# Performance work log

Hardware: AMD Instinct MI355X
Metric: run time of the kernel (lower is better)

The kernel has to match this reference:

```python
import jax, jax.numpy as jnp
import numpy as np

N_HEAD = 6


def setup_inputs() -> dict:
    key = jax.random.key(0)
    k1, k2, k3 = jax.random.split(key, 3)
    B, N, D = 16, 512, 768
    d_head = D // N_HEAD
    p_mask = jnp.ones((B, N), dtype=jnp.float32)
    feature = jax.random.normal(k1, (B, N, D), dtype=jnp.float32)
    # nn.Linear weights (out, in); scaled like torch default init
    W = jax.random.normal(k2, (D, D), dtype=jnp.float32) / np.sqrt(D)
    # attn Linear(2*d_head -> n_head); only the diagonal head rows are used
    Wa = jax.random.normal(k3, (N_HEAD, 2 * d_head), dtype=jnp.float32) / np.sqrt(2 * d_head)
    return {"p_mask": p_mask, "feature": feature, "W": W, "Wa": Wa, "num_layers": 2}


def reference(p_mask, feature, W, Wa, num_layers):
    B, N, D = feature.shape
    H = N_HEAD
    Dh = D // H
    # adj[b,q,k] = p_mask[b,q] * p_mask[b,k]  (bmm of unsqueezed mask)
    adj = p_mask[:, :, None] * p_mask[:, None, :]  # (B,N,N)
    mask = adj[:, :, :, None] > 0                   # (B,N,N,1)
    for _ in range(num_layers):
        residual = feature
        qk = (feature @ W.T).reshape(B, N, H, Dh)  # (B,N,H,Dh)
        # concat(q,k) @ Wa[h] decomposes into query part + key part
        sq = jnp.einsum('bqhd,hd->bqh', qk, Wa[:, :Dh])
        sk = jnp.einsum('bkhd,hd->bkh', qk, Wa[:, Dh:])
        score = jnp.tanh(sq[:, :, None, :] + sk[:, None, :, :])  # (B,N,N,H)
        # masked_fill with -1e-8 where adj == 0 (faithful to source)
        score = jnp.where(mask, score, jnp.float32(-1e-8))
        attn = jax.nn.softmax(score, axis=2)  # softmax over key dim (dim=-2)
        # dropout p=0 in eval -> identity
        hid = jnp.tanh(jnp.einsum('bqkh,bkhd->bqhd', attn, qk))  # (B,N,H,Dh)
        feature = residual + hid.reshape(B, N, D)
    return feature
```

## Files before the change

### kernel.cpp

```cpp
#include <hip/hip_runtime.h>
#include <hip/hip_bf16.h>
#include <stdint.h>

#define BATCH 16
#define NSEQ  512
#define DMODEL 768
#define NHEAD 6
#define DHEAD 128
#define MROWS (BATCH * NSEQ)
#define QBLK  32
#define KTILE 64

typedef __attribute__((ext_vector_type(8))) __bf16 bf16x8;
typedef __attribute__((ext_vector_type(4))) __bf16 bf16x4;
typedef __attribute__((ext_vector_type(4))) float  f32x4;
typedef __attribute__((ext_vector_type(4))) unsigned int u32x4;

#define GLD16(gp, lp) __builtin_amdgcn_global_load_lds( \
    (const __attribute__((address_space(1))) unsigned int*)(gp), \
    (__attribute__((address_space(3))) unsigned int*)(lp), 16, 0, 0)

#define BAR_PLAIN() do { asm volatile("" ::: "memory"); \
    __builtin_amdgcn_s_barrier(); asm volatile("" ::: "memory"); } while (0)
#define BAR_LGKM() do { asm volatile("s_waitcnt lgkmcnt(0)" ::: "memory"); \
    __builtin_amdgcn_s_barrier(); asm volatile("" ::: "memory"); } while (0)

__global__ void cvt_bf16_kernel(const float* __restrict__ src,
                                __bf16* __restrict__ dst, int n4) {
    int i = blockIdx.x * blockDim.x + threadIdx.x;
    if (i < n4) {
        float4 v = reinterpret_cast<const float4*>(src)[i];
        bf16x4 o;
        o.x = (__bf16)v.x; o.y = (__bf16)v.y; o.z = (__bf16)v.z; o.w = (__bf16)v.w;
        reinterpret_cast<bf16x4*>(dst)[i] = o;
    }
}

__global__ __launch_bounds__(256) void gemm_bt(const __bf16* __restrict__ A,
                                               const __bf16* __restrict__ Bm,
                                               __bf16* __restrict__ C,
                                               const float* __restrict__ Wa,
                                               const float* __restrict__ pmask,
                                               float* __restrict__ eq_t,
                                               float* __restrict__ ek_t) {
    __shared__ __align__(16) __bf16 As[2][64 * 32];
    __shared__ __align__(16) __bf16 Bs[2][128 * 32];
    const int tid  = threadIdx.x;
    const int lane = tid & 63;
    const int wave = tid >> 6;
    const int wm = wave >> 1, wn = wave & 1;

    const int wg  = blockIdx.x;
    const int nid = (wg & 7) * 96 + (wg >> 3);
    const int bx  = nid % 6;
    const int by  = nid / 6;
    const int m0 = by * 64;
    const int n0 = bx * 128;

    f32x4 acc[2][4] = {};

    const int e0   = tid * 8;
    const int row0 = tid >> 2;
    const int k0i  = (tid & 3) * 8;

    const int lr = lane & 15;
    const int lg = lane >> 4;
    const int kb = lg * 8;

    #define STAGE(kt, bufi) do { \
        GLD16(A  + (size_t)(m0 + row0)      * DMODEL + (kt) + k0i, &As[bufi][e0]); \
        GLD16(Bm + (size_t)(n0 + row0)      * DMODEL + (kt) + k0i, &Bs[bufi][e0]); \
        GLD16(Bm + (size_t)(n0 + row0 + 64) * DMODEL + (kt) + k0i, &Bs[bufi][e0 + 2048]); \
    } while (0)

    STAGE(0, 0);

    for (int t = 0; t < 24; t++) {
        const int buf = t & 1;
        if (t < 23) {
            STAGE((t + 1) * 32, buf ^ 1);
            asm volatile("s_waitcnt vmcnt(3)" ::: "memory");
        } else {
            asm volatile("s_waitcnt vmcnt(0)" ::: "memory");
        }
        __builtin_amdgcn_s_barrier();
        asm volatile("" ::: "memory");

        bf16x8 af[2], bfv[4];
        #pragma unroll
        for (int i = 0; i < 2; i++)
            af[i] = *reinterpret_cast<const bf16x8*>(&As[buf][(wm * 32 + i * 16 + lr) * 32 + kb]);
        #pragma unroll
        for (int j = 0; j < 4; j++)
            bfv[j] = *reinterpret_cast<const bf16x8*>(&Bs[buf][(wn * 64 + j * 16 + lr) * 32 + kb]);
        #pragma unroll
        for (int i = 0; i < 2; i++)
            #pragma unroll
            for (int j = 0; j < 4; j++)
                acc[i][j] = __builtin_amdgcn_mfma_f32_16x16x32_bf16(af[i], bfv[j], acc[i][j], 0, 0, 0);

        BAR_PLAIN();
    }
    #undef STAGE

    const int rg = lg * 4;
    #pragma unroll
    for (int i = 0; i < 2; i++) {
        #pragma unroll
        for (int j = 0; j < 4; j++) {
            #pragma unroll
            for (int r = 0; r < 4; r++) {
                int row = m0 + wm * 32 + i * 16 + rg + r;
                int col = n0 + wn * 64 + j * 16 + lr;
                C[(size_t)row * DMODEL + col] = (__bf16)acc[i][j][r];
            }
        }
    }

    const int h = bx;
    float wqv[4], wkv[4];
    #pragma unroll
    for (int j = 0; j < 4; j++) {
        int d = wn * 64 + j * 16 + lr;
        wqv[j] = Wa[h * 256 + d];
        wkv[j] = Wa[h * 256 + 128 + d];
    }
    float* red = reinterpret_cast<float*>(&As[0][0]);
    #pragma unroll
    for (int i = 0; i < 2; i++) {
        #pragma unroll
        for (int r = 0; r < 4; r++) {
            float aq = 0.f, ak = 0.f;
            #pragma unroll
            for (int j = 0; j < 4; j++) {
                aq += acc[i][j][r] * wqv[j];
                ak += acc[i][j][r] * wkv[j];
            }
            #pragma unroll
            for (int off = 1; off < 16; off <<= 1) {
                aq += __shfl_xor(aq, off);
                ak += __shfl_xor(ak, off);
            }
            if (lr == 0) {
                int row = wm * 32 + i * 16 + rg + r;
                red[(0 * 64 + row) * 2 + wn] = aq;
                red[(1 * 64 + row) * 2 + wn] = ak;
            }
        }
    }
    __syncthreads();
    if (tid < 64) {
        int row = m0 + tid;
        float s = red[tid * 2] + red[tid * 2 + 1];
        eq_t[(size_t)h * MROWS + row] = (pmask[row] > 0.f) ? __expf(2.f * s) : 0.f;
    } else if (tid < 128) {
        int rl  = tid - 64;
        int row = m0 + rl;
        float s = red[(64 + rl) * 2] + red[(64 + rl) * 2 + 1];
        ek_t[(size_t)h * MROWS + row] = (pmask[row] > 0.f) ? __expf(2.f * s) : 0.f;
    }
}

__global__ __launch_bounds__(256) void attn_pv(const __bf16* __restrict__ QK,
                                               const float* __restrict__ eq_t,
                                               const float* __restrict__ ek_t,
                                               const float* __restrict__ residual,
                                               float* __restrict__ out,
                                               __bf16* __restrict__ out_bf) {
    const int wg  = blockIdx.x;
    const int nid = (wg & 7) * 192 + (wg >> 3);
    const int qt = nid & 15;
    const int hb = nid >> 4;
    const int h  = hb % NHEAD;
    const int b  = hb / NHEAD;
    const int q0 = qt * QBLK;

    __shared__ __align__(16) __bf16 w[QBLK][512];
    __shared__ __align__(16) __bf16 Vt[2][DHEAD * KTILE];
    const int tid  = threadIdx.x;
    const int lane = tid & 63;
    const int wave = tid >> 6;

    const int wd0 = wave * 32;
    const int lr  = lane & 15;
    const int lg  = lane >> 4;

    const int sd0 = (tid & 15) * 8;
    const int sk0 = (tid >> 4) * 4;
    const __bf16* Vbase = QK + (size_t)b * NSEQ * DMODEL + (size_t)h * DHEAD + sd0;

    u32x4 A0, A1, A2, A3, B0, B1, B2, B3;
    #define LOADS(S0, S1, S2, S3, t) do { \
        const __bf16* p = Vbase + (size_t)((t) * KTILE + sk0) * DMODEL; \
        S0 = *reinterpret_cast<const u32x4*>(p); \
        S1 = *reinterpret_cast<const u32x4*>(p + DMODEL); \
        S2 = *reinterpret_cast<const u32x4*>(p + 2 * DMODEL); \
        S3 = *reinterpret_cast<const u32x4*>(p + 3 * DMODEL); \
    } while (0)
    #define WRITEV(S0, S1, S2, S3, bufi) do { \
        char* vtw = reinterpret_cast<char*>(&Vt[bufi][0]); \
        _Pragma("unroll") \
        for (int j = 0; j < 8; j++) { \
            int d = sd0 + j; \
            int swz = j ^ (tid & 7); \
            unsigned sel = (j & 1) ? 0x07060302u : 0x05040100u; \
            unsigned lo = __builtin_amdgcn_perm(S1[j >> 1], S0[j >> 1], sel); \
            unsigned hi = __builtin_amdgcn_perm(S3[j >> 1], S2[j >> 1], sel); \
            unsigned long long pk = (unsigned long long)lo | ((unsigned long long)hi << 32); \
            *reinterpret_cast<unsigned long long*>(vtw + d * 128 + ((sk0 ^ (swz << 3)) * 2)) = pk; \
        } \
    } while (0)

    LOADS(A0, A1, A2, A3, 0);
    LOADS(B0, B1, B2, B3, 1);

    float res[2][4][2];
    #pragma unroll
    for (int qh = 0; qh < 2; qh++) {
        #pragma unroll
        for (int r = 0; r < 4; r++) {
            int ql = qh * 16 + lg * 4 + r;
            #pragma unroll
            for (int n = 0; n < 2; n++) {
                int d = wd0 + n * 16 + lr;
                res[qh][r][n] = residual[((size_t)(b * NSEQ + q0 + ql)) * DMODEL + (size_t)h * DHEAD + d];
            }
        }
    }

    const int k0 = lane * 8;
    const size_t sbase = (size_t)h * MROWS + b * NSEQ;
    float4 e0v = *reinterpret_cast<const float4*>(&ek_t[sbase + k0]);
    float4 e1v = *reinterpret_cast<const float4*>(&ek_t[sbase + k0 + 4]);
    float ek[8] = {e0v.x, e0v.y, e0v.z, e0v.w, e1v.x, e1v.y, e1v.z, e1v.w};
    float eq[8];
    #pragma unroll
    for (int g = 0; g < 8; g++)
        eq[g] = eq_t[sbase + q0 + wave * 8 + g];

    WRITEV(A0, A1, A2, A3, 0);
    LOADS(A0, A1, A2, A3, 2);

    #pragma unroll
    for (int g = 0; g < 8; g++) {
        int q = wave * 8 + g;
        float eqv = eq[g];
        bf16x8 wv;
        #pragma unroll
        for (int j = 0; j < 8; j++) {
            float u = eqv * ek[j];
            float z = __builtin_amdgcn_rcpf(u + 1.f);
            float p = __expf(fmaf(z, -2.f, 1.f));
            wv[j] = (__bf16)(u > 0.f ? p : 1.0f);
        }
        *reinterpret_cast<bf16x8*>(&w[q][k0 ^ ((q & 7) << 3)]) = wv;
    }
    BAR_LGKM();

    bf16x8 vones;
    #pragma unroll
    for (int e = 0; e < 8; e++) vones[e] = (__bf16)1.0f;

    f32x4 acc[2][2] = {};
    f32x4 accs[2] = {};

    const int wswz = (lr & 7) << 3;

    #pragma unroll
    for (int t = 0; t < 8; t++) {
        const int buf = t & 1;
        const char* vtr = reinterpret_cast<const char*>(&Vt[buf][0]);
        if (t < 7) {
            if ((t & 1) == 0) WRITEV(B0, B1, B2, B3, buf ^ 1);
            else              WRITEV(A0, A1, A2, A3, buf ^ 1);
        }
        if (t < 5) {
            if ((t & 1) == 0) LOADS(B0, B1, B2, B3, t + 3);
            else              LOADS(A0, A1, A2, A3, t + 3);
        }
        __builtin_amdgcn_s_setprio(1);
        #pragma unroll
        for (int ks = 0; ks < 2; ks++) {
            int cb = (t * 64 + ks * 32 + lg * 8) ^ wswz;
            bf16x8 af0 = *reinterpret_cast<const bf16x8*>(&w[lr][cb]);
            bf16x8 af1 = *reinterpret_cast<const bf16x8*>(&w[16 + lr][cb]);
            #pragma unroll
            for (int n = 0; n < 2; n++) {
                int d    = wd0 + n * 16 + lr;
                int kbk  = ks * 4 + lg;
                int swzd = (d & 7) ^ ((d >> 3) & 7);
                bf16x8 bv = *reinterpret_cast<const bf16x8*>(vtr + d * 128 + ((kbk ^ swzd) << 4));
                acc[0][n] = __builtin_amdgcn_mfma_f32_16x16x32_bf16(af0, bv, acc[0][n], 0, 0, 0);
                acc[1][n] = __builtin_amdgcn_mfma_f32_16x16x32_bf16(af1, bv, acc[1][n], 0, 0, 0);
            }
            accs[0] = __builtin_amdgcn_mfma_f32_16x16x32_bf16(af0, vones, accs[0], 0, 0, 0);
            accs[1] = __builtin_amdgcn_mfma_f32_16x16x32_bf16(af1, vones, accs[1], 0, 0, 0);
        }
        __builtin_amdgcn_s_setprio(0);
        if (t < 7) BAR_LGKM();
    }

    #pragma unroll
    for (int qh = 0; qh < 2; qh++) {
        #pragma unroll
        for (int r = 0; r < 4; r++) {
            int ql = qh * 16 + lg * 4 + r;
            float rden = __builtin_amdgcn_rcpf(accs[qh][r]);
            #pragma unroll
            for (int n = 0; n < 2; n++) {
                int d  = wd0 + n * 16 + lr;
                float hv = acc[qh][n][r] * rden;
                float e2 = __expf(2.f * hv);
                float tv = 1.f - 2.f * __builtin_amdgcn_rcpf(e2 + 1.f);
                size_t o = ((size_t)(b * NSEQ + q0 + ql)) * DMODEL + (size_t)h * DHEAD + d;
                float ov = res[qh][r][n] + tv;
                out[o] = ov;
                if (out_bf) out_bf[o] = (__bf16)ov;
            }
        }
    }
    #undef LOADS
    #undef WRITEV
}

extern "C" void kernel_launch(void* const* d_in, const int* in_sizes, int n_in,
                              void* d_out, int out_size, void* d_ws, size_t ws_size,
                              hipStream_t stream) {
    const float* pmask   = (const float*)d_in[0];
    const float* feature = (const float*)d_in[1];
    const float* W       = (const float*)d_in[2];
    const float* Wa      = (const float*)d_in[3];
    float* out = (float*)d_out;
    char* ws = (char*)d_ws;

    __bf16* Abf  = (__bf16*)ws;
    __bf16* Wbf  = (__bf16*)(ws + 12582912);
    __bf16* QKbf = (__bf16*)(ws + 12582912 + 1179648);
    float*  eq   = (float*)(ws + 12582912 + 1179648 + 12582912);
    float*  ek   = eq + MROWS * NHEAD;

    const int featN4 = (MROWS * DMODEL) / 4;
    const int wN4    = (DMODEL * DMODEL) / 4;

    hipLaunchKernelGGL(cvt_bf16_kernel, dim3((wN4 + 255) / 256), dim3(256), 0, stream,
                       W, Wbf, wN4);

    hipLaunchKernelGGL(cvt_bf16_kernel, dim3((featN4 + 255) / 256), dim3(256), 0, stream,
                       feature, Abf, featN4);
    hipLaunchKernelGGL(gemm_bt, dim3(768), dim3(256), 0, stream,
                       Abf, Wbf, QKbf, Wa, pmask, eq, ek);
    hipLaunchKernelGGL(attn_pv, dim3(1536), dim3(256), 0, stream,
                       QKbf, eq, ek, feature, out, Abf);

    hipLaunchKernelGGL(gemm_bt, dim3(768), dim3(256), 0, stream,
                       Abf, Wbf, QKbf, Wa, pmask, eq, ek);
    hipLaunchKernelGGL(attn_pv, dim3(1536), dim3(256), 0, stream,
                       QKbf, eq, ek, out, out, (__bf16*)nullptr);
}
```

Baseline: 110.4 us.

## Fuse fp32-to-bf16 feature conversion into first GEMM and keep layer-1 output bf16

The first projection GEMM now loads fp32 feature rows directly and converts them to bf16 in registers before writing to LDS. This removes the separate full-size conversion kernel and its round trip through memory. Layer 1's attention output is now written only as bf16, not also as fp32, and layer 2 reads that bf16 buffer as its residual. Together these cut a large fp32 write and read, at the cost of a lower-precision residual carried into the final output and register-staged A loads in the fp32 GEMM variant.

```diff
diff --git a/kernel.cpp b/kernel.cpp
--- a/kernel.cpp
+++ b/kernel.cpp
@@ -36,13 +36,17 @@
     }
 }
 
-__global__ __launch_bounds__(256) void gemm_bt(const __bf16* __restrict__ A,
+template<bool AFP32>
+__global__ __launch_bounds__(256) void gemm_bt(const void* __restrict__ Av,
                                                const __bf16* __restrict__ Bm,
                                                __bf16* __restrict__ C,
                                                const float* __restrict__ Wa,
                                                const float* __restrict__ pmask,
                                                float* __restrict__ eq_t,
                                                float* __restrict__ ek_t) {
+    const __bf16* Ab = reinterpret_cast<const __bf16*>(Av);
+    const float*  Af = reinterpret_cast<const float*>(Av);
+
     __shared__ __align__(16) __bf16 As[2][64 * 32];
     __shared__ __align__(16) __bf16 Bs[2][128 * 32];
     const int tid  = threadIdx.x;
@@ -67,24 +71,65 @@
     const int lg = lane >> 4;
     const int kb = lg * 8;
 
-    #define STAGE(kt, bufi) do { \
-        GLD16(A  + (size_t)(m0 + row0)      * DMODEL + (kt) + k0i, &As[bufi][e0]); \
+    #define BSTAGE(kt, bufi) do { \
         GLD16(Bm + (size_t)(n0 + row0)      * DMODEL + (kt) + k0i, &Bs[bufi][e0]); \
         GLD16(Bm + (size_t)(n0 + row0 + 64) * DMODEL + (kt) + k0i, &Bs[bufi][e0 + 2048]); \
     } while (0)
-
-    STAGE(0, 0);
+    #define ALOADR(S0, S1, kt) do { \
+        const float* p = Af + (size_t)(m0 + row0) * DMODEL + (kt) + k0i; \
+        S0 = *reinterpret_cast<const float4*>(p); \
+        S1 = *reinterpret_cast<const float4*>(p + 4); \
+    } while (0)
+    #define AWRITE(S0, S1, bufi) do { \
+        bf16x8 v; \
+        v[0]=(__bf16)S0.x; v[1]=(__bf16)S0.y; v[2]=(__bf16)S0.z; v[3]=(__bf16)S0.w; \
+        v[4]=(__bf16)S1.x; v[5]=(__bf16)S1.y; v[6]=(__bf16)S1.z; v[7]=(__bf16)S1.w; \
+        *reinterpret_cast<bf16x8*>(&As[bufi][e0]) = v; \
+    } while (0)
+    #define STAGE_BF(kt, bufi) do { \
+        GLD16(Ab + (size_t)(m0 + row0)      * DMODEL + (kt) + k0i, &As[bufi][e0]); \
+        BSTAGE(kt, bufi); \
+    } while (0)
+
+    float4 X0, X1, Y0, Y1;
+
+    if constexpr (AFP32) {
+        ALOADR(X0, X1, 0);
+        ALOADR(Y0, Y1, 32);
+        BSTAGE(0, 0);
+        AWRITE(X0, X1, 0);
+        BAR_LGKM();
+    } else {
+        STAGE_BF(0, 0);
+    }
 
     for (int t = 0; t < 24; t++) {
         const int buf = t & 1;
-        if (t < 23) {
-            STAGE((t + 1) * 32, buf ^ 1);
-            asm volatile("s_waitcnt vmcnt(3)" ::: "memory");
+        if constexpr (AFP32) {
+            if (t < 23) BSTAGE((t + 1) * 32, buf ^ 1);
+            if (t < 22) {
+                if ((t & 1) == 0) ALOADR(X0, X1, (t + 2) * 32);
+                else              ALOADR(Y0, Y1, (t + 2) * 32);
+            }
+            if (t < 22)      asm volatile("s_waitcnt vmcnt(4)" ::: "memory");
+            else if (t < 23) asm volatile("s_waitcnt vmcnt(2)" ::: "memory");
+            else             asm volatile("s_waitcnt vmcnt(0)" ::: "memory");
+            __builtin_amdgcn_s_barrier();
+            asm volatile("" ::: "memory");
+            if (t < 23) {
+                if ((t & 1) == 0) AWRITE(Y0, Y1, buf ^ 1);
+                else              AWRITE(X0, X1, buf ^ 1);
+            }
         } else {
-            asm volatile("s_waitcnt vmcnt(0)" ::: "memory");
-        }
-        __builtin_amdgcn_s_barrier();
-        asm volatile("" ::: "memory");
+            if (t < 23) {
+                STAGE_BF((t + 1) * 32, buf ^ 1);
+                asm volatile("s_waitcnt vmcnt(3)" ::: "memory");
+            } else {
+                asm volatile("s_waitcnt vmcnt(0)" ::: "memory");
+            }
+            __builtin_amdgcn_s_barrier();
+            asm volatile("" ::: "memory");
+        }
 
         bf16x8 af[2], bfv[4];
         #pragma unroll
@@ -99,9 +144,13 @@
             for (int j = 0; j < 4; j++)
                 acc[i][j] = __builtin_amdgcn_mfma_f32_16x16x32_bf16(af[i], bfv[j], acc[i][j], 0, 0, 0);
 
-        BAR_PLAIN();
-    }
-    #undef STAGE
+        if constexpr (AFP32) BAR_LGKM();
+        else                 BAR_PLAIN();
+    }
+    #undef BSTAGE
+    #undef ALOADR
+    #undef AWRITE
+    #undef STAGE_BF
 
     const int rg = lg * 4;
     #pragma unroll
@@ -164,9 +213,10 @@
 __global__ __launch_bounds__(256) void attn_pv(const __bf16* __restrict__ QK,
                                                const float* __restrict__ eq_t,
                                                const float* __restrict__ ek_t,
-                                               const float* __restrict__ residual,
-                                               float* __restrict__ out,
-                                               __bf16* __restrict__ out_bf) {
+                                               const float* __restrict__ resf,
+                                               const __bf16* __restrict__ resb,
+                                               float* __restrict__ outf,
+                                               __bf16* __restrict__ outb) {
     const int wg  = blockIdx.x;
     const int nid = (wg & 7) * 192 + (wg >> 3);
     const int qt = nid & 15;
@@ -223,7 +273,8 @@
             #pragma unroll
             for (int n = 0; n < 2; n++) {
                 int d = wd0 + n * 16 + lr;
-                res[qh][r][n] = residual[((size_t)(b * NSEQ + q0 + ql)) * DMODEL + (size_t)h * DHEAD + d];
+                size_t o = ((size_t)(b * NSEQ + q0 + ql)) * DMODEL + (size_t)h * DHEAD + d;
+                res[qh][r][n] = resf ? resf[o] : (float)resb[o];
             }
         }
     }
@@ -314,8 +365,8 @@
                 float tv = 1.f - 2.f * __builtin_amdgcn_rcpf(e2 + 1.f);
                 size_t o = ((size_t)(b * NSEQ + q0 + ql)) * DMODEL + (size_t)h * DHEAD + d;
                 float ov = res[qh][r][n] + tv;
-                out[o] = ov;
-                if (out_bf) out_bf[o] = (__bf16)ov;
+                if (outf) outf[o] = ov;
+                if (outb) outb[o] = (__bf16)ov;
             }
         }
     }
@@ -339,21 +390,20 @@
     float*  eq   = (float*)(ws + 12582912 + 1179648 + 12582912);
     float*  ek   = eq + MROWS * NHEAD;
 
-    const int featN4 = (MROWS * DMODEL) / 4;
-    const int wN4    = (DMODEL * DMODEL) / 4;
+    const int wN4 = (DMODEL * DMODEL) / 4;
 
     hipLaunchKernelGGL(cvt_bf16_kernel, dim3((wN4 + 255) / 256), dim3(256), 0, stream,
                        W, Wbf, wN4);
 
-    hipLaunchKernelGGL(cvt_bf16_kernel, dim3((featN4 + 255) / 256), dim3(256), 0, stream,
-                       feature, Abf, featN4);
-    hipLaunchKernelGGL(gemm_bt, dim3(768), dim3(256), 0, stream,
-                       Abf, Wbf, QKbf, Wa, pmask, eq, ek);
+    hipLaunchKernelGGL((gemm_bt<true>), dim3(768), dim3(256), 0, stream,
+                       (const void*)feature, Wbf, QKbf, Wa, pmask, eq, ek);
     hipLaunchKernelGGL(attn_pv, dim3(1536), dim3(256), 0, stream,
-                       QKbf, eq, ek, feature, out, Abf);
-
-    hipLaunchKernelGGL(gemm_bt, dim3(768), dim3(256), 0, stream,
-                       Abf, Wbf, QKbf, Wa, pmask, eq, ek);
+                       QKbf, eq, ek, feature, (const __bf16*)nullptr,
+                       (float*)nullptr, Abf);
+
+    hipLaunchKernelGGL((gemm_bt<false>), dim3(768), dim3(256), 0, stream,
+                       (const void*)Abf, Wbf, QKbf, Wa, pmask, eq, ek);
     hipLaunchKernelGGL(attn_pv, dim3(1536), dim3(256), 0, stream,
-                       QKbf, eq, ek, out, out, (__bf16*)nullptr);
+                       QKbf, eq, ek, (const float*)nullptr, Abf,
+                       out, (__bf16*)nullptr);
 }
```

New measurement: 114.8 us. 4.0% more time.

## Merge bf16 conversions and pass layer-1 residual as bf16 only

Applied to the files above, without the earlier changes.

The two fp32-to-bf16 conversion launches become one kernel that handles both the weight and the feature ranges, removing a launch. The first attention layer now writes only the bf16 feature, no longer an fp32 copy, and the second layer reads its residual from that bf16 buffer. This cuts global memory traffic between layers. The cost is that the residual carried into layer two loses precision, which could push error past tolerance.

```diff
diff --git a/kernel.cpp b/kernel.cpp
--- a/kernel.cpp
+++ b/kernel.cpp
@@ -25,15 +25,18 @@
 #define BAR_LGKM() do { asm volatile("s_waitcnt lgkmcnt(0)" ::: "memory"); \
     __builtin_amdgcn_s_barrier(); asm volatile("" ::: "memory"); } while (0)
 
-__global__ void cvt_bf16_kernel(const float* __restrict__ src,
-                                __bf16* __restrict__ dst, int n4) {
+__global__ void cvt_bf16_dual(const float* __restrict__ srcA, __bf16* __restrict__ dstA, int n4A,
+                              const float* __restrict__ srcB, __bf16* __restrict__ dstB, int n4B) {
     int i = blockIdx.x * blockDim.x + threadIdx.x;
-    if (i < n4) {
-        float4 v = reinterpret_cast<const float4*>(src)[i];
-        bf16x4 o;
-        o.x = (__bf16)v.x; o.y = (__bf16)v.y; o.z = (__bf16)v.z; o.w = (__bf16)v.w;
-        reinterpret_cast<bf16x4*>(dst)[i] = o;
-    }
+    const float* s;
+    __bf16* d;
+    int idx;
+    if (i < n4A) { s = srcA; d = dstA; idx = i; }
+    else         { idx = i - n4A; if (idx >= n4B) return; s = srcB; d = dstB; }
+    float4 v = reinterpret_cast<const float4*>(s)[idx];
+    bf16x4 o;
+    o.x = (__bf16)v.x; o.y = (__bf16)v.y; o.z = (__bf16)v.z; o.w = (__bf16)v.w;
+    reinterpret_cast<bf16x4*>(d)[idx] = o;
 }
 
 __global__ __launch_bounds__(256) void gemm_bt(const __bf16* __restrict__ A,
@@ -161,12 +164,14 @@
     }
 }
 
+template<int LAYER>
 __global__ __launch_bounds__(256) void attn_pv(const __bf16* __restrict__ QK,
                                                const float* __restrict__ eq_t,
                                                const float* __restrict__ ek_t,
-                                               const float* __restrict__ residual,
-                                               float* __restrict__ out,
-                                               __bf16* __restrict__ out_bf) {
+                                               const float* __restrict__ resf,
+                                               const __bf16* __restrict__ resb,
+                                               float* __restrict__ outf,
+                                               __bf16* __restrict__ outb) {
     const int wg  = blockIdx.x;
     const int nid = (wg & 7) * 192 + (wg >> 3);
     const int qt = nid & 15;
@@ -223,7 +228,9 @@
             #pragma unroll
             for (int n = 0; n < 2; n++) {
                 int d = wd0 + n * 16 + lr;
-                res[qh][r][n] = residual[((size_t)(b * NSEQ + q0 + ql)) * DMODEL + (size_t)h * DHEAD + d];
+                size_t o = ((size_t)(b * NSEQ + q0 + ql)) * DMODEL + (size_t)h * DHEAD + d;
+                if constexpr (LAYER == 0) res[qh][r][n] = resf[o];
+                else                      res[qh][r][n] = (float)resb[o];
             }
         }
     }
@@ -314,8 +321,8 @@
                 float tv = 1.f - 2.f * __builtin_amdgcn_rcpf(e2 + 1.f);
                 size_t o = ((size_t)(b * NSEQ + q0 + ql)) * DMODEL + (size_t)h * DHEAD + d;
                 float ov = res[qh][r][n] + tv;
-                out[o] = ov;
-                if (out_bf) out_bf[o] = (__bf16)ov;
+                if constexpr (LAYER == 0) outb[o] = (__bf16)ov;
+                else                      outf[o] = ov;
             }
         }
     }
@@ -339,21 +346,21 @@
     float*  eq   = (float*)(ws + 12582912 + 1179648 + 12582912);
     float*  ek   = eq + MROWS * NHEAD;
 
+    const int wN4    = (DMODEL * DMODEL) / 4;
     const int featN4 = (MROWS * DMODEL) / 4;
-    const int wN4    = (DMODEL * DMODEL) / 4;
-
-    hipLaunchKernelGGL(cvt_bf16_kernel, dim3((wN4 + 255) / 256), dim3(256), 0, stream,
-                       W, Wbf, wN4);
-
-    hipLaunchKernelGGL(cvt_bf16_kernel, dim3((featN4 + 255) / 256), dim3(256), 0, stream,
-                       feature, Abf, featN4);
+
+    hipLaunchKernelGGL(cvt_bf16_dual, dim3((wN4 + featN4 + 255) / 256), dim3(256), 0, stream,
+                       W, Wbf, wN4, feature, Abf, featN4);
+
     hipLaunchKernelGGL(gemm_bt, dim3(768), dim3(256), 0, stream,
                        Abf, Wbf, QKbf, Wa, pmask, eq, ek);
-    hipLaunchKernelGGL(attn_pv, dim3(1536), dim3(256), 0, stream,
-                       QKbf, eq, ek, feature, out, Abf);
+    hipLaunchKernelGGL((attn_pv<0>), dim3(1536), dim3(256), 0, stream,
+                       QKbf, eq, ek, feature, (const __bf16*)nullptr,
+                       (float*)nullptr, Abf);
 
     hipLaunchKernelGGL(gemm_bt, dim3(768), dim3(256), 0, stream,
                        Abf, Wbf, QKbf, Wa, pmask, eq, ek);
-    hipLaunchKernelGGL(attn_pv, dim3(1536), dim3(256), 0, stream,
-                       QKbf, eq, ek, out, out, (__bf16*)nullptr);
+    hipLaunchKernelGGL((attn_pv<1>), dim3(1536), dim3(256), 0, stream,
+                       QKbf, eq, ek, (const float*)nullptr, Abf,
+                       out, (__bf16*)nullptr);
 }
```

Result: faster. 103.5 us (-6.2%).
